# Optimization experiments

Measured on AMD Instinct MI355X. Metric: run time of the kernel, lower is better.

Reference implementation:

```python
import jax, jax.numpy as jnp
import numpy as np

HEADS = 16
HEAD_DIM = 64
EMBED = HEADS * HEAD_DIM  # 1024
B, S = 2, 2048


def setup_inputs() -> dict:
    key = jax.random.key(0)
    ks = jax.random.split(key, 9)
    return {
        "value": jax.random.normal(ks[0], (B, S, EMBED), dtype=jnp.float32),
        "key": jax.random.normal(ks[1], (B, S, EMBED), dtype=jnp.float32),
        "query": jax.random.normal(ks[2], (B, S, EMBED), dtype=jnp.float32),
        "mask": jax.random.randint(ks[3], (B, 1, S, S), 0, 2, dtype=jnp.int32),
        "Wq": jax.random.normal(ks[4], (HEAD_DIM, HEAD_DIM), dtype=jnp.float32) * 0.02,
        "Wk": jax.random.normal(ks[5], (HEAD_DIM, HEAD_DIM), dtype=jnp.float32) * 0.02,
        "Wv": jax.random.normal(ks[6], (HEAD_DIM, HEAD_DIM), dtype=jnp.float32) * 0.02,
        "Wo": jax.random.normal(ks[7], (EMBED, EMBED), dtype=jnp.float32) * 0.02,
        "bo": jnp.zeros((EMBED,), dtype=jnp.float32),
    }


def reference(value, key, query, mask, Wq, Wk, Wv, Wo, bo):
    N, Lv = value.shape[0], value.shape[1]
    Lk, Lq = key.shape[1], query.shape[1]
    # Faithful to original: plain reshape (N, heads, len, head_dim), NOT transpose.
    v = value.reshape(N, HEADS, Lv, HEAD_DIM)
    k = key.reshape(N, HEADS, Lk, HEAD_DIM)
    q = query.reshape(N, HEADS, Lq, HEAD_DIM)
    # Per-head Linear (no bias): x @ W.T
    V = jnp.einsum('bhld,ed->bhle', v, Wv)
    K = jnp.einsum('bhld,ed->bhle', k, Wk)
    Q = jnp.einsum('bhld,ed->bhle', q, Wq)
    score = jnp.einsum('bhqd,bhkd->bhqk', Q, K)  # [B,H,Sq,Sk]
    score = jnp.where(mask == 0, jnp.float32(-1e20), score)
    # Faithful quirk: scale by sqrt(embed_size), not sqrt(head_dim)
    scale = jnp.float32(EMBED ** 0.5)
    attn = jax.nn.softmax(score / scale, axis=3)
    out = jnp.einsum('bhqk,bhkd->bhqd', attn, V).reshape(N, Lq, HEADS * HEAD_DIM)
    return out @ Wo.T + bo
```

## Files before the change

### kernel.cpp

```cpp
#include <hip/hip_runtime.h>
#include <hip/hip_bf16.h>
#include <cstdint>
#include <cstddef>

#define S_LEN 2048
#define N_HEADS 16
#define HD 64
#define EMB 1024
#define N_BATCH 2
#define N_BH (N_BATCH * N_HEADS)

typedef __attribute__((ext_vector_type(4))) float f32x4;
typedef __attribute__((ext_vector_type(8))) short short8;
typedef __attribute__((ext_vector_type(8))) _Float16 half8;
typedef __attribute__((ext_vector_type(2))) unsigned uint2v;
typedef __attribute__((ext_vector_type(4))) unsigned uint4v;

__device__ __forceinline__ f32x4 mfma16h(half8 a, half8 b, f32x4 c) {
    return __builtin_amdgcn_mfma_f32_16x16x32_f16(a, b, c, 0, 0, 0);
}

__device__ __forceinline__ unsigned pkh(float a, float b) {
    return __builtin_bit_cast(unsigned, __builtin_amdgcn_cvt_pkrtz(a, b));
}

#if __has_builtin(__builtin_amdgcn_exp2f)
__device__ __forceinline__ float fast_exp2(float x) { return __builtin_amdgcn_exp2f(x); }
#else
__device__ __forceinline__ float fast_exp2(float x) { return exp2f(x); }
#endif

__global__ __launch_bounds__(256) void prep_kernel(
    const float* __restrict__ q_in, const float* __restrict__ k_in,
    const float* __restrict__ v_in,
    const float* __restrict__ Wq, const float* __restrict__ Wk,
    const float* __restrict__ Wv, const float* __restrict__ Wo,
    const int* __restrict__ mask,
    short* __restrict__ Qb, short* __restrict__ Kb, short* __restrict__ Vt,
    short* __restrict__ Woh, unsigned long long* __restrict__ bits) {
    __shared__ short Al[64 * 72];
    __shared__ short Wl[64 * 72];
    __shared__ short Ol[64 * 72];
    int bx = blockIdx.x;
    int t = threadIdx.x;

    if (bx >= 3072) {
        if (bx < 11264) {
            int wid = ((bx - 3072) * 256 + t) >> 6;
            int lane = t & 63;
            const int* src = mask + (size_t)wid * 256 + lane;
            unsigned long long w0 = __ballot(src[0] != 0);
            unsigned long long w1 = __ballot(src[64] != 0);
            unsigned long long w2 = __ballot(src[128] != 0);
            unsigned long long w3 = __ballot(src[192] != 0);
            if (lane == 0) {
                unsigned long long* dst = bits + (size_t)wid * 4;
                dst[0] = w0; dst[1] = w1; dst[2] = w2; dst[3] = w3;
            }
        } else {
            int i = (bx - 11264) * 256 + t;
            f32x4 a = reinterpret_cast<const f32x4*>(Wo)[i * 2];
            f32x4 b = reinterpret_cast<const f32x4*>(Wo)[i * 2 + 1];
            uint4 u = { pkh(a.x, a.y), pkh(a.z, a.w), pkh(b.x, b.y), pkh(b.z, b.w) };
            reinterpret_cast<uint4*>(Woh)[i] = u;
        }
        return;
    }

    int rt = bx & 31;
    int bh = (bx >> 5) & 31;
    int tz = bx >> 10;
    const float* src = (tz == 0 ? q_in : tz == 1 ? k_in : v_in)
                       + (size_t)bh * S_LEN * HD + (size_t)rt * 64 * HD;
    const float* W = (tz == 0 ? Wq : tz == 1 ? Wk : Wv);

#pragma unroll
    for (int r = 0; r < 4; r++) {
        int f4 = t + 256 * r;
        int row = f4 >> 4;
        int c4 = (f4 & 15) * 4;
        f32x4 a = reinterpret_cast<const f32x4*>(src)[f4];
        uint2 ua = { pkh(a.x, a.y), pkh(a.z, a.w) };
        *reinterpret_cast<uint2*>(&Al[row * 72 + c4]) = ua;
        f32x4 w = reinterpret_cast<const f32x4*>(W)[f4];
        uint2 uw = { pkh(w.x, w.y), pkh(w.z, w.w) };
        *reinterpret_cast<uint2*>(&Wl[row * 72 + c4]) = uw;
    }
    __syncthreads();

    int wave = t >> 6, lane = t & 63, quad = lane >> 4, col = lane & 15;
    half8 a0 = *reinterpret_cast<const half8*>(&Al[(wave * 16 + col) * 72 + quad * 8]);
    half8 a1 = *reinterpret_cast<const half8*>(&Al[(wave * 16 + col) * 72 + 32 + quad * 8]);

    const float C1 = 0.04508422002777448f;
    float scl = (tz == 0) ? C1 : 1.0f;

    f32x4 acc[4];
#pragma unroll
    for (int jt = 0; jt < 4; jt++) {
        half8 b0 = *reinterpret_cast<const half8*>(&Wl[(jt * 16 + col) * 72 + quad * 8]);
        half8 b1 = *reinterpret_cast<const half8*>(&Wl[(jt * 16 + col) * 72 + 32 + quad * 8]);
        f32x4 c = {0.f, 0.f, 0.f, 0.f};
        c = mfma16h(a0, b0, c);
        c = mfma16h(a1, b1, c);
        acc[jt] = c;
    }
    __syncthreads();

    if (tz < 2) {
#pragma unroll
        for (int jt = 0; jt < 4; jt++)
#pragma unroll
            for (int i = 0; i < 4; i++)
                Ol[(wave * 16 + quad * 4 + i) * 72 + jt * 16 + col] =
                    __builtin_bit_cast(short, (_Float16)(acc[jt][i] * scl));
        __syncthreads();
        short* dst = (tz == 0 ? Qb : Kb) + (size_t)bh * S_LEN * HD + (size_t)rt * 64 * HD;
        int row = t >> 2, ck = (t & 3) * 16;
        short8 o0 = *reinterpret_cast<const short8*>(&Ol[row * 72 + ck]);
        short8 o1 = *reinterpret_cast<const short8*>(&Ol[row * 72 + ck + 8]);
        *reinterpret_cast<short8*>(&dst[row * 64 + ck]) = o0;
        *reinterpret_cast<short8*>(&dst[row * 64 + ck + 8]) = o1;
    } else {
#pragma unroll
        for (int jt = 0; jt < 4; jt++)
#pragma unroll
            for (int i = 0; i < 4; i++)
                Ol[(jt * 16 + col) * 72 + wave * 16 + quad * 4 + i] =
                    __builtin_bit_cast(short, (_Float16)acc[jt][i]);
        __syncthreads();
        short* dst = Vt + (size_t)bh * HD * S_LEN + rt * 64;
        int d = t >> 2, ck = (t & 3) * 16;
        short8 o0 = *reinterpret_cast<const short8*>(&Ol[d * 72 + ck]);
        short8 o1 = *reinterpret_cast<const short8*>(&Ol[d * 72 + ck + 8]);
        *reinterpret_cast<short8*>(&dst[(size_t)d * S_LEN + ck]) = o0;
        *reinterpret_cast<short8*>(&dst[(size_t)d * S_LEN + ck + 8]) = o1;
    }
}

__global__ __launch_bounds__(512, 4) void attn_kernel(
    const short* __restrict__ Qb, const short* __restrict__ Kb,
    const short* __restrict__ Vt, const unsigned long long* __restrict__ mbits,
    short* __restrict__ Xb) {
    int qt = blockIdx.x;
    int bh = blockIdx.y;
    int b = bh >> 4;
    int t = threadIdx.x, wave = t >> 6, lane = t & 63, quad = lane >> 4, col = lane & 15;
    int qg = wave & 3;
    int par = wave >> 2;

    __shared__ short smem[16384 + 9216 + 256];
    const short* Kp = smem + par * 4096;
    const short* Vp = smem + 8192 + par * 4096;

    const short* Qh = Qb + (size_t)bh * S_LEN * HD;
    const short* Kh = Kb + (size_t)bh * S_LEN * HD;
    const short* Vh = Vt + (size_t)bh * HD * S_LEN;
    int q0 = qt * 128 + qg * 32;

    half8 qf00 = *reinterpret_cast<const half8*>(&Qh[(size_t)(q0 + col) * HD + quad * 8]);
    half8 qf01 = *reinterpret_cast<const half8*>(&Qh[(size_t)(q0 + col) * HD + 32 + quad * 8]);
    half8 qf10 = *reinterpret_cast<const half8*>(&Qh[(size_t)(q0 + 16 + col) * HD + quad * 8]);
    half8 qf11 = *reinterpret_cast<const half8*>(&Qh[(size_t)(q0 + 16 + col) * HD + 32 + quad * 8]);

    const unsigned long long* mrow0 = mbits + (size_t)(b * S_LEN + q0 + col) * 32;
    const unsigned long long* mrow1 = mbits + (size_t)(b * S_LEN + q0 + 16 + col) * 32;

    int r0 = t >> 3, cc = t & 7;
    int dst0 = r0 * 64 + ((cc ^ (r0 & 7)) * 8);
    int ch0 = cc & ~1;
    int h4 = (cc & 1) * 4;
    int vdA = r0 * 64 + ((ch0 ^ (r0 & 7)) * 8) + h4;
    int vdB = r0 * 64 + (((ch0 + 1) ^ (r0 & 7)) * 8) + h4;
    const short* kg0 = Kh + r0 * HD + cc * 8;
    const short* vg0 = Vh + (size_t)r0 * S_LEN + cc * 8;

    {
        short8 a = *reinterpret_cast<const short8*>(kg0);
        short8 b2 = *reinterpret_cast<const short8*>(kg0 + 4096);
        uint4v uc = __builtin_bit_cast(uint4v, *reinterpret_cast<const short8*>(vg0));
        uint4v ud = __builtin_bit_cast(uint4v, *reinterpret_cast<const short8*>(vg0 + 64));
        *reinterpret_cast<short8*>(&smem[dst0]) = a;
        *reinterpret_cast<short8*>(&smem[4096 + dst0]) = b2;
        *reinterpret_cast<uint2v*>(&smem[8192 + vdA]) = (uint2v){uc.x, uc.y};
        *reinterpret_cast<uint2v*>(&smem[8192 + vdB]) = (uint2v){uc.z, uc.w};
        *reinterpret_cast<uint2v*>(&smem[12288 + vdA]) = (uint2v){ud.x, ud.y};
        *reinterpret_cast<uint2v*>(&smem[12288 + vdB]) = (uint2v){ud.z, ud.w};
    }
    __syncthreads();

    unsigned bs[4];
#pragma unroll
    for (int i = 0; i < 4; i++) bs[i] = 1u << (quad * 4 + i);
    half8 ones = { (_Float16)1.f, (_Float16)1.f, (_Float16)1.f, (_Float16)1.f,
                   (_Float16)1.f, (_Float16)1.f, (_Float16)1.f, (_Float16)1.f };

    int sw = quad ^ (col & 7);
    unsigned long long mw0 = mrow0[par];
    unsigned long long mw1 = mrow1[par];

    f32x4 o[4][2];
    f32x4 l0 = {0.f, 0.f, 0.f, 0.f}, l1 = {0.f, 0.f, 0.f, 0.f};
#pragma unroll
    for (int dt = 0; dt < 4; dt++) {
        o[dt][0] = (f32x4){0.f, 0.f, 0.f, 0.f};
        o[dt][1] = (f32x4){0.f, 0.f, 0.f, 0.f};
    }

    for (int s = 0; s < 16; s++) {
        short8 pk0, pk1, pv0, pv1;
        unsigned long long mn0, mn1;
        if (s < 15) {
            pk0 = *reinterpret_cast<const short8*>(kg0 + (2 * s + 2) * 4096);
            pk1 = *reinterpret_cast<const short8*>(kg0 + (2 * s + 3) * 4096);
            pv0 = *reinterpret_cast<const short8*>(vg0 + (2 * s + 2) * 64);
            pv1 = *reinterpret_cast<const short8*>(vg0 + (2 * s + 3) * 64);
            mn0 = mrow0[2 * s + 2 + par];
            mn1 = mrow1[2 * s + 2 + par];
        }
        unsigned wA[4][2], wB[4][2];
#pragma unroll
        for (int mt = 0; mt < 4; mt++) {
            const short* kbase = &Kp[(mt * 16 + col) * 64];
            half8 ka0 = *reinterpret_cast<const half8*>(&kbase[sw * 8]);
            half8 ka1 = *reinterpret_cast<const half8*>(&kbase[(sw ^ 4) * 8]);
            f32x4 c0 = {0.f, 0.f, 0.f, 0.f};
            f32x4 c1 = {0.f, 0.f, 0.f, 0.f};
            c0 = mfma16h(ka0, qf00, c0);
            c0 = mfma16h(ka1, qf01, c0);
            c1 = mfma16h(ka0, qf10, c1);
            c1 = mfma16h(ka1, qf11, c1);
            unsigned g0 = (unsigned)(mw0 >> (mt * 16));
            unsigned g1 = (unsigned)(mw1 >> (mt * 16));
            float p00 = fast_exp2((g0 & bs[0]) ? c0[0] : -200.0f);
            float p01 = fast_exp2((g0 & bs[1]) ? c0[1] : -200.0f);
            float p02 = fast_exp2((g0 & bs[2]) ? c0[2] : -200.0f);
            float p03 = fast_exp2((g0 & bs[3]) ? c0[3] : -200.0f);
            wA[mt][0] = pkh(p00, p01);
            wA[mt][1] = pkh(p02, p03);
            float p10 = fast_exp2((g1 & bs[0]) ? c1[0] : -200.0f);
            float p11 = fast_exp2((g1 & bs[1]) ? c1[1] : -200.0f);
            float p12 = fast_exp2((g1 & bs[2]) ? c1[2] : -200.0f);
            float p13 = fast_exp2((g1 & bs[3]) ? c1[3] : -200.0f);
            wB[mt][0] = pkh(p10, p11);
            wB[mt][1] = pkh(p12, p13);
        }
#pragma unroll
        for (int c = 0; c < 2; c++) {
            auto ra0 = __builtin_amdgcn_permlane32_swap(wA[2 * c][0], wA[2 * c + 1][0], false, false);
            auto ra1 = __builtin_amdgcn_permlane32_swap(wA[2 * c][1], wA[2 * c + 1][1], false, false);
            auto rb0 = __builtin_amdgcn_permlane32_swap(wB[2 * c][0], wB[2 * c + 1][0], false, false);
            auto rb1 = __builtin_amdgcn_permlane32_swap(wB[2 * c][1], wB[2 * c + 1][1], false, false);
            half8 pb0 = __builtin_bit_cast(half8, (uint4v){ra0[0], ra1[0], ra0[1], ra1[1]});
            half8 pb1 = __builtin_bit_cast(half8, (uint4v){rb0[0], rb1[0], rb0[1], rb1[1]});
            l0 = mfma16h(ones, pb0, l0);
            l1 = mfma16h(ones, pb1, l1);
#pragma unroll
            for (int dt = 0; dt < 4; dt++) {
                half8 va = *reinterpret_cast<const half8*>(
                    &Vp[(dt * 16 + col) * 64 + (((c * 4 + quad) ^ (col & 7)) * 8)]);
                o[dt][0] = mfma16h(va, pb0, o[dt][0]);
                o[dt][1] = mfma16h(va, pb1, o[dt][1]);
            }
        }
        __syncthreads();
        if (s < 15) {
            uint4v u0 = __builtin_bit_cast(uint4v, pv0);
            uint4v u1 = __builtin_bit_cast(uint4v, pv1);
            *reinterpret_cast<short8*>(&smem[dst0]) = pk0;
            *reinterpret_cast<short8*>(&smem[4096 + dst0]) = pk1;
            *reinterpret_cast<uint2v*>(&smem[8192 + vdA]) = (uint2v){u0.x, u0.y};
            *reinterpret_cast<uint2v*>(&smem[8192 + vdB]) = (uint2v){u0.z, u0.w};
            *reinterpret_cast<uint2v*>(&smem[12288 + vdA]) = (uint2v){u1.x, u1.y};
            *reinterpret_cast<uint2v*>(&smem[12288 + vdB]) = (uint2v){u1.z, u1.w};
            mw0 = mn0;
            mw1 = mn1;
            __syncthreads();
        }
    }

    float* Obuf = (float*)smem;
    short* Ps = smem + 16384;
    float* Lbuf = (float*)(smem + 16384 + 9216);
    if (par == 1) {
        float* ob = Obuf + qg * 2048 + lane * 32;
#pragma unroll
        for (int dt = 0; dt < 4; dt++) {
            *reinterpret_cast<f32x4*>(&ob[((dt * 2 + 0) ^ (lane & 7)) * 4]) = o[dt][0];
            *reinterpret_cast<f32x4*>(&ob[((dt * 2 + 1) ^ (lane & 7)) * 4]) = o[dt][1];
        }
        if (quad == 0) {
            Lbuf[qg * 32 + col] = l0[0];
            Lbuf[qg * 32 + 16 + col] = l1[0];
        }
    }
    __syncthreads();
    if (par == 0) {
        short* Pw = Ps + qg * (32 * 72);
        float* ob = Obuf + qg * 2048 + lane * 32;
        float inv0 = 1.0f / (l0[0] + Lbuf[qg * 32 + col]);
        float inv1 = 1.0f / (l1[0] + Lbuf[qg * 32 + 16 + col]);
#pragma unroll
        for (int dt = 0; dt < 4; dt++) {
            f32x4 a0 = *reinterpret_cast<const f32x4*>(&ob[((dt * 2 + 0) ^ (lane & 7)) * 4]);
            f32x4 a1 = *reinterpret_cast<const f32x4*>(&ob[((dt * 2 + 1) ^ (lane & 7)) * 4]);
            float v00 = (o[dt][0][0] + a0.x) * inv0, v01 = (o[dt][0][1] + a0.y) * inv0;
            float v02 = (o[dt][0][2] + a0.z) * inv0, v03 = (o[dt][0][3] + a0.w) * inv0;
            float v10 = (o[dt][1][0] + a1.x) * inv1, v11 = (o[dt][1][1] + a1.y) * inv1;
            float v12 = (o[dt][1][2] + a1.z) * inv1, v13 = (o[dt][1][3] + a1.w) * inv1;
            uint2 dw0 = { pkh(v00, v01), pkh(v02, v03) };
            uint2 dw1 = { pkh(v10, v11), pkh(v12, v13) };
            *reinterpret_cast<uint2*>(&Pw[col * 72 + dt * 16 + quad * 4]) = dw0;
            *reinterpret_cast<uint2*>(&Pw[(16 + col) * 72 + dt * 16 + quad * 4]) = dw1;
        }
        int rr = lane >> 2, ckk = (lane & 3) * 16;
        short* Xrow = Xb + (size_t)bh * S_LEN * HD + (size_t)(q0 + rr) * HD;
        short8 x0 = *reinterpret_cast<const short8*>(&Pw[rr * 72 + ckk]);
        short8 x1 = *reinterpret_cast<const short8*>(&Pw[rr * 72 + ckk + 8]);
        *reinterpret_cast<short8*>(&Xrow[ckk]) = x0;
        *reinterpret_cast<short8*>(&Xrow[ckk + 8]) = x1;
        short* Xrow2 = Xrow + 16 * HD;
        short8 y0 = *reinterpret_cast<const short8*>(&Pw[(16 + rr) * 72 + ckk]);
        short8 y1 = *reinterpret_cast<const short8*>(&Pw[(16 + rr) * 72 + ckk + 8]);
        *reinterpret_cast<short8*>(&Xrow2[ckk]) = y0;
        *reinterpret_cast<short8*>(&Xrow2[ckk + 8]) = y1;
    }
}

__global__ __launch_bounds__(256, 4) void final_kernel(
    const short* __restrict__ Xb, const short* __restrict__ Woh,
    const float* __restrict__ bo, float* __restrict__ out) {
    int nb = blockIdx.x;
    int mb = blockIdx.y;
    int t = threadIdx.x, wave = t >> 6, lane = t & 63, quad = lane >> 4, col = lane & 15;
    __shared__ short Xs[128 * 64];
    __shared__ short Ws[64 * 64];

    int m0 = mb * 128, n0 = nb * 64;
    int r0 = t >> 3, cc = t & 7;

    int dstX[4], dstW[2];
    const short* xg[4];
    const short* wg[2];
#pragma unroll
    for (int u = 0; u < 4; u++) {
        int row = r0 + u * 32;
        dstX[u] = row * 64 + ((cc ^ (row & 7)) * 8);
        xg[u] = Xb + (size_t)(m0 + row) * EMB + cc * 8;
    }
#pragma unroll
    for (int u = 0; u < 2; u++) {
        int row = r0 + u * 32;
        dstW[u] = row * 64 + ((cc ^ (row & 7)) * 8);
        wg[u] = Woh + (size_t)(n0 + row) * EMB + cc * 8;
    }

    short8 px[4], pw[2];
#pragma unroll
    for (int u = 0; u < 4; u++) px[u] = *reinterpret_cast<const short8*>(xg[u]);
#pragma unroll
    for (int u = 0; u < 2; u++) pw[u] = *reinterpret_cast<const short8*>(wg[u]);
#pragma unroll
    for (int u = 0; u < 4; u++) *reinterpret_cast<short8*>(&Xs[dstX[u]]) = px[u];
#pragma unroll
    for (int u = 0; u < 2; u++) *reinterpret_cast<short8*>(&Ws[dstW[u]]) = pw[u];
    __syncthreads();

    int sw = quad ^ (col & 7);
    f32x4 acc[2][4];
#pragma unroll
    for (int mf = 0; mf < 2; mf++)
#pragma unroll
        for (int nf = 0; nf < 4; nf++) acc[mf][nf] = (f32x4){0.f, 0.f, 0.f, 0.f};

    for (int s = 0; s < 16; s++) {
        if (s < 15) {
#pragma unroll
            for (int u = 0; u < 4; u++)
                px[u] = *reinterpret_cast<const short8*>(xg[u] + (s + 1) * 64);
#pragma unroll
            for (int u = 0; u < 2; u++)
                pw[u] = *reinterpret_cast<const short8*>(wg[u] + (s + 1) * 64);
        }
        const short* ar0 = &Xs[(wave * 32 + col) * 64];
        const short* ar1 = &Xs[(wave * 32 + 16 + col) * 64];
        half8 a00 = *reinterpret_cast<const half8*>(&ar0[sw * 8]);
        half8 a01 = *reinterpret_cast<const half8*>(&ar0[(sw ^ 4) * 8]);
        half8 a10 = *reinterpret_cast<const half8*>(&ar1[sw * 8]);
        half8 a11 = *reinterpret_cast<const half8*>(&ar1[(sw ^ 4) * 8]);
#pragma unroll
        for (int nf = 0; nf < 4; nf++) {
            const short* br = &Ws[(nf * 16 + col) * 64];
            half8 b0 = *reinterpret_cast<const half8*>(&br[sw * 8]);
            half8 b1 = *reinterpret_cast<const half8*>(&br[(sw ^ 4) * 8]);
            acc[0][nf] = mfma16h(a00, b0, acc[0][nf]);
            acc[0][nf] = mfma16h(a01, b1, acc[0][nf]);
            acc[1][nf] = mfma16h(a10, b0, acc[1][nf]);
            acc[1][nf] = mfma16h(a11, b1, acc[1][nf]);
        }
        __syncthreads();
        if (s < 15) {
#pragma unroll
            for (int u = 0; u < 4; u++) *reinterpret_cast<short8*>(&Xs[dstX[u]]) = px[u];
#pragma unroll
            for (int u = 0; u < 2; u++) *reinterpret_cast<short8*>(&Ws[dstW[u]]) = pw[u];
            __syncthreads();
        }
    }

    float bb[4];
#pragma unroll
    for (int nf = 0; nf < 4; nf++) bb[nf] = bo[n0 + nf * 16 + col];
#pragma unroll
    for (int mf = 0; mf < 2; mf++)
#pragma unroll
        for (int i = 0; i < 4; i++) {
            int row = m0 + wave * 32 + mf * 16 + quad * 4 + i;
            float* orow = out + (size_t)row * EMB + n0;
#pragma unroll
            for (int nf = 0; nf < 4; nf++)
                orow[nf * 16 + col] = acc[mf][nf][i] + bb[nf];
        }
}

extern "C" void kernel_launch(void* const* d_in, const int* in_sizes, int n_in,
                              void* d_out, int out_size, void* d_ws, size_t ws_size,
                              hipStream_t stream) {
    const float* value = (const float*)d_in[0];
    const float* key_  = (const float*)d_in[1];
    const float* query = (const float*)d_in[2];
    const int*   mask  = (const int*)d_in[3];
    const float* Wq = (const float*)d_in[4];
    const float* Wk = (const float*)d_in[5];
    const float* Wv = (const float*)d_in[6];
    const float* Wo = (const float*)d_in[7];
    const float* bo = (const float*)d_in[8];
    float* out = (float*)d_out;

    char* ws = (char*)d_ws;
    short* Qb  = (short*)(ws);
    short* Kb  = (short*)(ws + (size_t)8  * 1048576);
    short* Vt  = (short*)(ws + (size_t)16 * 1048576);
    short* Xb  = (short*)(ws + (size_t)24 * 1048576);
    short* Woh = (short*)(ws + (size_t)32 * 1048576);
    unsigned long long* mbits =
        (unsigned long long*)(ws + (size_t)34 * 1048576);

    prep_kernel<<<dim3(3072 + 8192 + 512), dim3(256), 0, stream>>>(
        query, key_, value, Wq, Wk, Wv, Wo, mask, Qb, Kb, Vt, Woh, mbits);
    attn_kernel<<<dim3(S_LEN / 128, N_BH), dim3(512), 0, stream>>>(Qb, Kb, Vt, mbits, Xb);
    final_kernel<<<dim3(EMB / 64, (N_BATCH * S_LEN) / 128), dim3(256), 0, stream>>>(
        Xb, Woh, bo, out);
}
```

Before: 200.2 us.

## Halve attention block to 64 queries with 256 threads, add MFMA priority hints

The attention kernel now uses 256-thread blocks, each covering 64 query rows instead of 128, which doubles the grid and shrinks shared memory. That should raise occupancy and improve load balance across CUs. Each thread now loads twice as many K/V elements per tile, and K/V global traffic doubles because each tile is shared by fewer queries. s_setprio hints are also placed around the MFMA sections so other waves' memory work can interleave with them.

```diff
diff --git a/kernel.cpp b/kernel.cpp
--- a/kernel.cpp
+++ b/kernel.cpp
@@ -138,7 +138,7 @@
     }
 }
 
-__global__ __launch_bounds__(512, 4) void attn_kernel(
+__global__ __launch_bounds__(256, 4) void attn_kernel(
     const short* __restrict__ Qb, const short* __restrict__ Kb,
     const short* __restrict__ Vt, const unsigned long long* __restrict__ mbits,
     short* __restrict__ Xb) {
@@ -146,17 +146,17 @@
     int bh = blockIdx.y;
     int b = bh >> 4;
     int t = threadIdx.x, wave = t >> 6, lane = t & 63, quad = lane >> 4, col = lane & 15;
-    int qg = wave & 3;
-    int par = wave >> 2;
-
-    __shared__ short smem[16384 + 9216 + 256];
+    int qg = wave & 1;
+    int par = wave >> 1;
+
+    __shared__ short smem[16384];
     const short* Kp = smem + par * 4096;
     const short* Vp = smem + 8192 + par * 4096;
 
     const short* Qh = Qb + (size_t)bh * S_LEN * HD;
     const short* Kh = Kb + (size_t)bh * S_LEN * HD;
     const short* Vh = Vt + (size_t)bh * HD * S_LEN;
-    int q0 = qt * 128 + qg * 32;
+    int q0 = qt * 64 + qg * 32;
 
     half8 qf00 = *reinterpret_cast<const half8*>(&Qh[(size_t)(q0 + col) * HD + quad * 8]);
     half8 qf01 = *reinterpret_cast<const half8*>(&Qh[(size_t)(q0 + col) * HD + 32 + quad * 8]);
@@ -174,18 +174,29 @@
     int vdB = r0 * 64 + (((ch0 + 1) ^ (r0 & 7)) * 8) + h4;
     const short* kg0 = Kh + r0 * HD + cc * 8;
     const short* vg0 = Vh + (size_t)r0 * S_LEN + cc * 8;
+    const int VROW2 = 32 * S_LEN;
 
     {
-        short8 a = *reinterpret_cast<const short8*>(kg0);
-        short8 b2 = *reinterpret_cast<const short8*>(kg0 + 4096);
-        uint4v uc = __builtin_bit_cast(uint4v, *reinterpret_cast<const short8*>(vg0));
-        uint4v ud = __builtin_bit_cast(uint4v, *reinterpret_cast<const short8*>(vg0 + 64));
-        *reinterpret_cast<short8*>(&smem[dst0]) = a;
-        *reinterpret_cast<short8*>(&smem[4096 + dst0]) = b2;
-        *reinterpret_cast<uint2v*>(&smem[8192 + vdA]) = (uint2v){uc.x, uc.y};
-        *reinterpret_cast<uint2v*>(&smem[8192 + vdB]) = (uint2v){uc.z, uc.w};
-        *reinterpret_cast<uint2v*>(&smem[12288 + vdA]) = (uint2v){ud.x, ud.y};
-        *reinterpret_cast<uint2v*>(&smem[12288 + vdB]) = (uint2v){ud.z, ud.w};
+        short8 a0 = *reinterpret_cast<const short8*>(kg0);
+        short8 a1 = *reinterpret_cast<const short8*>(kg0 + 2048);
+        short8 b0 = *reinterpret_cast<const short8*>(kg0 + 4096);
+        short8 b1 = *reinterpret_cast<const short8*>(kg0 + 4096 + 2048);
+        uint4v c0 = __builtin_bit_cast(uint4v, *reinterpret_cast<const short8*>(vg0));
+        uint4v c1 = __builtin_bit_cast(uint4v, *reinterpret_cast<const short8*>(vg0 + VROW2));
+        uint4v d0 = __builtin_bit_cast(uint4v, *reinterpret_cast<const short8*>(vg0 + 64));
+        uint4v d1 = __builtin_bit_cast(uint4v, *reinterpret_cast<const short8*>(vg0 + 64 + VROW2));
+        *reinterpret_cast<short8*>(&smem[dst0]) = a0;
+        *reinterpret_cast<short8*>(&smem[dst0 + 2048]) = a1;
+        *reinterpret_cast<short8*>(&smem[4096 + dst0]) = b0;
+        *reinterpret_cast<short8*>(&smem[4096 + dst0 + 2048]) = b1;
+        *reinterpret_cast<uint2v*>(&smem[8192 + vdA]) = (uint2v){c0.x, c0.y};
+        *reinterpret_cast<uint2v*>(&smem[8192 + vdB]) = (uint2v){c0.z, c0.w};
+        *reinterpret_cast<uint2v*>(&smem[8192 + vdA + 2048]) = (uint2v){c1.x, c1.y};
+        *reinterpret_cast<uint2v*>(&smem[8192 + vdB + 2048]) = (uint2v){c1.z, c1.w};
+        *reinterpret_cast<uint2v*>(&smem[12288 + vdA]) = (uint2v){d0.x, d0.y};
+        *reinterpret_cast<uint2v*>(&smem[12288 + vdB]) = (uint2v){d0.z, d0.w};
+        *reinterpret_cast<uint2v*>(&smem[12288 + vdA + 2048]) = (uint2v){d1.x, d1.y};
+        *reinterpret_cast<uint2v*>(&smem[12288 + vdB + 2048]) = (uint2v){d1.z, d1.w};
     }
     __syncthreads();
 
@@ -208,13 +219,21 @@
     }
 
     for (int s = 0; s < 16; s++) {
-        short8 pk0, pk1, pv0, pv1;
+        short8 pk0, pk0b, pk1, pk1b, pv0, pv0b, pv1, pv1b;
         unsigned long long mn0, mn1;
         if (s < 15) {
-            pk0 = *reinterpret_cast<const short8*>(kg0 + (2 * s + 2) * 4096);
-            pk1 = *reinterpret_cast<const short8*>(kg0 + (2 * s + 3) * 4096);
-            pv0 = *reinterpret_cast<const short8*>(vg0 + (2 * s + 2) * 64);
-            pv1 = *reinterpret_cast<const short8*>(vg0 + (2 * s + 3) * 64);
+            const short* ka = kg0 + (2 * s + 2) * 4096;
+            const short* kb = kg0 + (2 * s + 3) * 4096;
+            const short* va = vg0 + (2 * s + 2) * 64;
+            const short* vb = vg0 + (2 * s + 3) * 64;
+            pk0 = *reinterpret_cast<const short8*>(ka);
+            pk0b = *reinterpret_cast<const short8*>(ka + 2048);
+            pk1 = *reinterpret_cast<const short8*>(kb);
+            pk1b = *reinterpret_cast<const short8*>(kb + 2048);
+            pv0 = *reinterpret_cast<const short8*>(va);
+            pv0b = *reinterpret_cast<const short8*>(va + VROW2);
+            pv1 = *reinterpret_cast<const short8*>(vb);
+            pv1b = *reinterpret_cast<const short8*>(vb + VROW2);
             mn0 = mrow0[2 * s + 2 + par];
             mn1 = mrow1[2 * s + 2 + par];
         }
@@ -226,10 +245,12 @@
             half8 ka1 = *reinterpret_cast<const half8*>(&kbase[(sw ^ 4) * 8]);
             f32x4 c0 = {0.f, 0.f, 0.f, 0.f};
             f32x4 c1 = {0.f, 0.f, 0.f, 0.f};
+            __builtin_amdgcn_s_setprio(1);
             c0 = mfma16h(ka0, qf00, c0);
             c0 = mfma16h(ka1, qf01, c0);
             c1 = mfma16h(ka0, qf10, c1);
             c1 = mfma16h(ka1, qf11, c1);
+            __builtin_amdgcn_s_setprio(0);
             unsigned g0 = (unsigned)(mw0 >> (mt * 16));
             unsigned g1 = (unsigned)(mw1 >> (mt * 16));
             float p00 = fast_exp2((g0 & bs[0]) ? c0[0] : -200.0f);
@@ -253,6 +274,7 @@
             auto rb1 = __builtin_amdgcn_permlane32_swap(wB[2 * c][1], wB[2 * c + 1][1], false, false);
             half8 pb0 = __builtin_bit_cast(half8, (uint4v){ra0[0], ra1[0], ra0[1], ra1[1]});
             half8 pb1 = __builtin_bit_cast(half8, (uint4v){rb0[0], rb1[0], rb0[1], rb1[1]});
+            __builtin_amdgcn_s_setprio(1);
             l0 = mfma16h(ones, pb0, l0);
             l1 = mfma16h(ones, pb1, l1);
 #pragma unroll
@@ -262,17 +284,26 @@
                 o[dt][0] = mfma16h(va, pb0, o[dt][0]);
                 o[dt][1] = mfma16h(va, pb1, o[dt][1]);
             }
+            __builtin_amdgcn_s_setprio(0);
         }
         __syncthreads();
         if (s < 15) {
             uint4v u0 = __builtin_bit_cast(uint4v, pv0);
+            uint4v u0b = __builtin_bit_cast(uint4v, pv0b);
             uint4v u1 = __builtin_bit_cast(uint4v, pv1);
+            uint4v u1b = __builtin_bit_cast(uint4v, pv1b);
             *reinterpret_cast<short8*>(&smem[dst0]) = pk0;
+            *reinterpret_cast<short8*>(&smem[dst0 + 2048]) = pk0b;
             *reinterpret_cast<short8*>(&smem[4096 + dst0]) = pk1;
+            *reinterpret_cast<short8*>(&smem[4096 + dst0 + 2048]) = pk1b;
             *reinterpret_cast<uint2v*>(&smem[8192 + vdA]) = (uint2v){u0.x, u0.y};
             *reinterpret_cast<uint2v*>(&smem[8192 + vdB]) = (uint2v){u0.z, u0.w};
+            *reinterpret_cast<uint2v*>(&smem[8192 + vdA + 2048]) = (uint2v){u0b.x, u0b.y};
+            *reinterpret_cast<uint2v*>(&smem[8192 + vdB + 2048]) = (uint2v){u0b.z, u0b.w};
             *reinterpret_cast<uint2v*>(&smem[12288 + vdA]) = (uint2v){u1.x, u1.y};
             *reinterpret_cast<uint2v*>(&smem[12288 + vdB]) = (uint2v){u1.z, u1.w};
+            *reinterpret_cast<uint2v*>(&smem[12288 + vdA + 2048]) = (uint2v){u1b.x, u1b.y};
+            *reinterpret_cast<uint2v*>(&smem[12288 + vdB + 2048]) = (uint2v){u1b.z, u1b.w};
             mw0 = mn0;
             mw1 = mn1;
             __syncthreads();
@@ -280,8 +311,8 @@
     }
 
     float* Obuf = (float*)smem;
-    short* Ps = smem + 16384;
-    float* Lbuf = (float*)(smem + 16384 + 9216);
+    short* Ps = smem + 8192;
+    float* Lbuf = (float*)(smem + 8192 + 4608);
     if (par == 1) {
         float* ob = Obuf + qg * 2048 + lane * 32;
 #pragma unroll
@@ -448,7 +479,7 @@
 
     prep_kernel<<<dim3(3072 + 8192 + 512), dim3(256), 0, stream>>>(
         query, key_, value, Wq, Wk, Wv, Wo, mask, Qb, Kb, Vt, Woh, mbits);
-    attn_kernel<<<dim3(S_LEN / 128, N_BH), dim3(512), 0, stream>>>(Qb, Kb, Vt, mbits, Xb);
+    attn_kernel<<<dim3(S_LEN / 64, N_BH), dim3(256), 0, stream>>>(Qb, Kb, Vt, mbits, Xb);
     final_kernel<<<dim3(EMB / 64, (N_BATCH * S_LEN) / 128), dim3(256), 0, stream>>>(
         Xb, Woh, bo, out);
 }
```

Result: slower. 253.2 us (+26.5%).
